# Performance work log

Hardware: AMD Instinct MI355X
Metric: run time of the kernel (lower is better)

## Reference

```python
import jax, jax.numpy as jnp
import numpy as np

N_NODES = 50000
N_EDGES = 800000
F_IN = 256
HID = 128
HEADS = 4
F_OUT = 64
NEG_SLOPE = 0.2


def setup_inputs() -> dict:
    key = jax.random.key(0)
    ks = jax.random.split(key, 12)
    x = jax.random.normal(ks[0], (N_NODES, F_IN), dtype=jnp.float32)
    edge_index = jax.random.randint(ks[1], (2, N_EDGES), 0, N_NODES, dtype=jnp.int64)
    s = 0.05
    return {
        "x": x,
        "edge_index": edge_index,
        "W1": jax.random.normal(ks[2], (F_IN, HEADS * HID), dtype=jnp.float32) * s,
        "a_src1": jax.random.normal(ks[3], (HEADS, HID), dtype=jnp.float32) * s,
        "a_dst1": jax.random.normal(ks[4], (HEADS, HID), dtype=jnp.float32) * s,
        "b1": jnp.zeros((HEADS * HID,), dtype=jnp.float32),
        "W2": jax.random.normal(ks[5], (HEADS * HID, F_OUT), dtype=jnp.float32) * s,
        "a_src2": jax.random.normal(ks[6], (1, F_OUT), dtype=jnp.float32) * s,
        "a_dst2": jax.random.normal(ks[7], (1, F_OUT), dtype=jnp.float32) * s,
        "b2": jnp.zeros((F_OUT,), dtype=jnp.float32),
    }


def _add_self_loops(edge_index, n):
    loop = jnp.arange(n, dtype=edge_index.dtype)
    return jnp.concatenate([edge_index, jnp.stack([loop, loop])], axis=1)


def _gat_conv(x, edge_index, W, a_src, a_dst, bias, heads, out_ch):
    # PyG GATConv: h = x @ W reshaped to [N, H, C]
    n = x.shape[0]
    h = (x @ W).reshape(n, heads, out_ch)
    # per-node attention logits [N, H]
    al_src = jnp.einsum('nhc,hc->nh', h, a_src)
    al_dst = jnp.einsum('nhc,hc->nh', h, a_dst)
    src, dst = edge_index[0], edge_index[1]
    e = jax.nn.leaky_relu(al_src[src] + al_dst[dst], NEG_SLOPE)  # [E, H]
    # softmax over incoming edges per destination node (segment softmax)
    e_max = jax.ops.segment_max(e, dst, num_segments=n)
    e_exp = jnp.exp(e - e_max[dst])
    denom = jax.ops.segment_sum(e_exp, dst, num_segments=n)
    alpha = e_exp / (denom[dst] + 1e-16)  # [E, H]
    msg = h[src] * alpha[:, :, None]  # [E, H, C]
    out = jax.ops.segment_sum(msg, dst, num_segments=n)  # [N, H, C]
    return out.reshape(n, heads * out_ch) + bias


def reference(x, edge_index, W1, a_src1, a_dst1, b1, W2, a_src2, a_dst2, b2):
    # Dropout layers are identity in eval mode.
    ei = _add_self_loops(edge_index, x.shape[0])
    h = jax.nn.elu(_gat_conv(x, ei, W1, a_src1, a_dst1, b1, HEADS, HID))
    out = _gat_conv(h, ei, W2, a_src2, a_dst2, b2, 1, F_OUT)
    return out
```

## Files before the change

### kernel.cpp

```cpp
#include <hip/hip_runtime.h>
#include <math.h>

#define N_NODES 50000
#define N_EDGES 800000
#define E_TOT   850000
#define F_IN    256
#define F1      512
#define HID     128
#define HEADS   4
#define F_OUT   64

typedef __attribute__((ext_vector_type(8))) short short8;
typedef __attribute__((ext_vector_type(4))) float f32x4;
typedef unsigned short ushort_t;
typedef unsigned int uint_t;

__device__ __forceinline__ float lrelu(float x){ return x > 0.f ? x : 0.2f*x; }
__device__ __forceinline__ float elu(float x){ return x > 0.f ? x : expm1f(x); }

__device__ __forceinline__ ushort_t f2b(float f){
  uint_t u = __builtin_bit_cast(uint_t, f);
  u += 0x7fffu + ((u >> 16) & 1u);
  return (ushort_t)(u >> 16);
}
__device__ __forceinline__ float blo(uint_t u){ return __builtin_bit_cast(float, u << 16); }
__device__ __forceinline__ float bhi(uint_t u){ return __builtin_bit_cast(float, u & 0xffff0000u); }
__device__ __forceinline__ float b2f(ushort_t s){ return __builtin_bit_cast(float, (uint_t)s << 16); }

__global__ void hist_kernel(const int* __restrict__ ei, int* __restrict__ deg){
  int e = blockIdx.x*blockDim.x + threadIdx.x;
  if (e >= E_TOT) return;
  int dst = (e < N_EDGES) ? ei[N_EDGES + e] : (e - N_EDGES);
  atomicAdd(&deg[dst], 1);
}

__global__ __launch_bounds__(256) void scan1_kernel(const int* __restrict__ deg,
                                                    int* __restrict__ offs,
                                                    int* __restrict__ bsum){
  __shared__ int sd[256];
  const int tid = threadIdx.x;
  const int i = blockIdx.x*256 + tid;
  int v = (i < N_NODES) ? deg[i] : 0;
  sd[tid] = v; __syncthreads();
  #pragma unroll
  for (int off = 1; off < 256; off <<= 1){
    int t = (tid >= off) ? sd[tid - off] : 0;
    __syncthreads();
    sd[tid] += t;
    __syncthreads();
  }
  if (i < N_NODES) offs[i] = sd[tid] - v;
  if (tid == 255) bsum[blockIdx.x] = sd[255];
}

__global__ __launch_bounds__(256) void scan2_kernel(const int* __restrict__ bsum,
                                                    int* __restrict__ bbase, int nb){
  __shared__ int sd[256];
  const int tid = threadIdx.x;
  int v = (tid < nb) ? bsum[tid] : 0;
  sd[tid] = v; __syncthreads();
  #pragma unroll
  for (int off = 1; off < 256; off <<= 1){
    int t = (tid >= off) ? sd[tid - off] : 0;
    __syncthreads();
    sd[tid] += t;
    __syncthreads();
  }
  if (tid < nb) bbase[tid] = sd[tid] - v;
}

__global__ __launch_bounds__(256) void scan3_kernel(int* __restrict__ offs,
                                                    const int* __restrict__ bbase,
                                                    int* __restrict__ cur){
  const int i = blockIdx.x*256 + threadIdx.x;
  if (i < N_NODES){
    int o = offs[i] + bbase[blockIdx.x];
    offs[i] = o;
    cur[i] = o;
  }
  if (blockIdx.x == 0 && threadIdx.x == 0) offs[N_NODES] = E_TOT;
}

__global__ void scatter_kernel(const int* __restrict__ ei, int* __restrict__ cur,
                               int* __restrict__ ssrc){
  int e = blockIdx.x*blockDim.x + threadIdx.x;
  if (e >= E_TOT) return;
  int src, dst;
  if (e < N_EDGES){ src = ei[e]; dst = ei[N_EDGES + e]; }
  else            { src = e - N_EDGES; dst = src; }
  int pos = atomicAdd(&cur[dst], 1);
  ssrc[pos] = src;
}

__global__ __launch_bounds__(256) void cvt_x_kernel(const float* __restrict__ x,
                                                    ushort_t* __restrict__ xb){
  const int t = blockIdx.x*256 + threadIdx.x;
  const float4 a = ((const float4*)x)[t*2];
  const float4 b = ((const float4*)x)[t*2 + 1];
  uint4 o;
  o.x = (uint_t)f2b(a.x) | ((uint_t)f2b(a.y) << 16);
  o.y = (uint_t)f2b(a.z) | ((uint_t)f2b(a.w) << 16);
  o.z = (uint_t)f2b(b.x) | ((uint_t)f2b(b.y) << 16);
  o.w = (uint_t)f2b(b.z) | ((uint_t)f2b(b.w) << 16);
  ((uint4*)xb)[t] = o;
}

__global__ __launch_bounds__(256) void transpose_bf16_kernel(const float* __restrict__ W,
                                                             ushort_t* __restrict__ Wt,
                                                             int K, int N){
  __shared__ float tile[64][65];
  const int k0 = blockIdx.x*64, n0 = blockIdx.y*64;
  const int c = threadIdx.x & 63, r4 = threadIdx.x >> 6;
  for (int r = r4; r < 64; r += 4)
    tile[r][c] = W[(size_t)(k0 + r)*N + n0 + c];
  __syncthreads();
  for (int r = r4; r < 64; r += 4)
    Wt[(size_t)(n0 + r)*K + k0 + c] = f2b(tile[c][r]);
}

template<int K, int WR, int WC>
__global__ __launch_bounds__(256) void gemm_bf16(const ushort_t* __restrict__ A,
                                                 const ushort_t* __restrict__ Bt,
                                                 ushort_t* __restrict__ C,
                                                 int M, int N){
  constexpr int BM = WR*64, BN = WC*64, BKP = 40;
  __shared__ ushort_t As[BM*BKP];
  __shared__ ushort_t Bs[BN*BKP];
  const int tid = threadIdx.x;
  const int wave = tid >> 6, lane = tid & 63, quad = lane >> 4, l16 = lane & 15;
  const int wm = wave % WR, wn = wave / WR;
  const int m0 = blockIdx.x*BM, n0 = blockIdx.y*BN;
  f32x4 acc[4][4] = {};
  for (int k0 = 0; k0 < K; k0 += 32){
    #pragma unroll
    for (int s = tid; s < BM*4; s += 256){
      int r = s >> 2, c = s & 3;
      int gr = m0 + r; if (gr >= M) gr = M - 1;
      *(uint4*)(As + r*BKP + c*8) = *(const uint4*)(A + (size_t)gr*K + k0 + c*8);
    }
    #pragma unroll
    for (int s = tid; s < BN*4; s += 256){
      int r = s >> 2, c = s & 3;
      *(uint4*)(Bs + r*BKP + c*8) = *(const uint4*)(Bt + (size_t)(n0 + r)*K + k0 + c*8);
    }
    __syncthreads();
    short8 af[4], bfr[4];
    #pragma unroll
    for (int i = 0; i < 4; ++i)
      af[i] = *(const short8*)(As + (wm*64 + i*16 + l16)*BKP + quad*8);
    #pragma unroll
    for (int j = 0; j < 4; ++j)
      bfr[j] = *(const short8*)(Bs + (wn*64 + j*16 + l16)*BKP + quad*8);
    #pragma unroll
    for (int i = 0; i < 4; ++i)
      #pragma unroll
      for (int j = 0; j < 4; ++j)
        acc[i][j] = __builtin_amdgcn_mfma_f32_16x16x32_bf16(af[i], bfr[j], acc[i][j], 0, 0, 0);
    __syncthreads();
  }
  #pragma unroll
  for (int i = 0; i < 4; ++i){
    #pragma unroll
    for (int r = 0; r < 4; ++r){
      int row = m0 + wm*64 + i*16 + quad*4 + r;
      if (row < M){
        #pragma unroll
        for (int j = 0; j < 4; ++j){
          int col = n0 + wn*64 + j*16 + l16;
          C[(size_t)row*N + col] = f2b(acc[i][j][r]);
        }
      }
    }
  }
}

__global__ __launch_bounds__(128) void logits1_kernel(const ushort_t* __restrict__ h1b,
                                                      const float* __restrict__ a_src,
                                                      const float* __restrict__ a_dst,
                                                      float* __restrict__ als,
                                                      float* __restrict__ ald){
  const int n = blockIdx.x;
  const int tid = threadIdx.x;
  const int head = tid >> 5, p = tid & 31;
  const uint2 v = *(const uint2*)(h1b + (size_t)n*F1 + tid*4);
  float h0 = blo(v.x), h1 = bhi(v.x), h2 = blo(v.y), h3 = bhi(v.y);
  const float4 as = *(const float4*)(a_src + head*HID + p*4);
  const float4 ad = *(const float4*)(a_dst + head*HID + p*4);
  float ds = h0*as.x + h1*as.y + h2*as.z + h3*as.w;
  float dd = h0*ad.x + h1*ad.y + h2*ad.z + h3*ad.w;
  #pragma unroll
  for (int off = 16; off >= 1; off >>= 1){
    ds += __shfl_down(ds, off, 32);
    dd += __shfl_down(dd, off, 32);
  }
  if (p == 0){ als[n*4 + head] = ds; ald[n*4 + head] = dd; }
}

#define FMA8(hv, al) do{ \
  acc[0] = fmaf(blo((hv).x), (al), acc[0]); \
  acc[1] = fmaf(bhi((hv).x), (al), acc[1]); \
  acc[2] = fmaf(blo((hv).y), (al), acc[2]); \
  acc[3] = fmaf(bhi((hv).y), (al), acc[3]); \
  acc[4] = fmaf(blo((hv).z), (al), acc[4]); \
  acc[5] = fmaf(bhi((hv).z), (al), acc[5]); \
  acc[6] = fmaf(blo((hv).w), (al), acc[6]); \
  acc[7] = fmaf(bhi((hv).w), (al), acc[7]); }while(0)

__global__ __launch_bounds__(256) void agg1_kernel(const ushort_t* __restrict__ h1b,
                                                   const float* __restrict__ als,
                                                   const float* __restrict__ ald1,
                                                   const float* __restrict__ b1,
                                                   const int* __restrict__ offs,
                                                   const int* __restrict__ ssrc,
                                                   ushort_t* __restrict__ hb){
  __shared__ int   shsrc[4][64];
  __shared__ float shal[4][64][4];
  const int wave = threadIdx.x >> 6, lane = threadIdx.x & 63;
  const int n = blockIdx.x*4 + wave;
  const int head = lane >> 4;
  const float4 ald = ((const float4*)ald1)[n];
  const int s0 = offs[n], s1 = offs[n+1];
  const int nE = s1 - s0;

  float acc[8] = {0.f,0.f,0.f,0.f,0.f,0.f,0.f,0.f};

  if (nE <= 64){
    float4 a4 = {0.f,0.f,0.f,0.f};
    int sc = 0;
    if (lane < nE){
      sc = ssrc[s0 + lane];
      const float4 as = ((const float4*)als)[sc];
      a4.x = __expf(lrelu(as.x + ald.x));
      a4.y = __expf(lrelu(as.y + ald.y));
      a4.z = __expf(lrelu(as.z + ald.z));
      a4.w = __expf(lrelu(as.w + ald.w));
    }
    shsrc[wave][lane] = sc;
    *(float4*)&shal[wave][lane][0] = a4;

    const ushort_t* hbase = h1b + lane*8;
    const int nE4 = (nE + 3) & ~3;
    float dsum = 0.f;

    uint4 h0  = *(const uint4*)(hbase + ((size_t)shsrc[wave][0] << 9));
    uint4 h1v = *(const uint4*)(hbase + ((size_t)shsrc[wave][1] << 9));
    uint4 h2v = *(const uint4*)(hbase + ((size_t)shsrc[wave][2] << 9));
    uint4 h3v = *(const uint4*)(hbase + ((size_t)shsrc[wave][3] << 9));
    float al0 = shal[wave][0][head];
    float al1 = shal[wave][1][head];
    float al2 = shal[wave][2][head];
    float al3 = shal[wave][3][head];
    for (int k = 0; k < nE4; k += 4){
      uint4 p0 = h0, p1 = h1v, p2 = h2v, p3 = h3v;
      float q0 = 0.f, q1 = 0.f, q2 = 0.f, q3 = 0.f;
      if (k + 4 < nE4){
        p0 = *(const uint4*)(hbase + ((size_t)shsrc[wave][k+4] << 9));
        p1 = *(const uint4*)(hbase + ((size_t)shsrc[wave][k+5] << 9));
        p2 = *(const uint4*)(hbase + ((size_t)shsrc[wave][k+6] << 9));
        p3 = *(const uint4*)(hbase + ((size_t)shsrc[wave][k+7] << 9));
        q0 = shal[wave][k+4][head];
        q1 = shal[wave][k+5][head];
        q2 = shal[wave][k+6][head];
        q3 = shal[wave][k+7][head];
      }
      dsum += (al0 + al1) + (al2 + al3);
      FMA8(h0,  al0);
      FMA8(h1v, al1);
      FMA8(h2v, al2);
      FMA8(h3v, al3);
      h0 = p0; h1v = p1; h2v = p2; h3v = p3;
      al0 = q0; al1 = q1; al2 = q2; al3 = q3;
    }

    const float rd = 1.0f / (dsum + 1e-16f);
    const float4 ba = *(const float4*)(b1 + lane*8);
    const float4 bb = *(const float4*)(b1 + lane*8 + 4);
    float o0 = elu(fmaf(acc[0], rd, ba.x)), o1 = elu(fmaf(acc[1], rd, ba.y));
    float o2 = elu(fmaf(acc[2], rd, ba.z)), o3 = elu(fmaf(acc[3], rd, ba.w));
    float o4 = elu(fmaf(acc[4], rd, bb.x)), o5 = elu(fmaf(acc[5], rd, bb.y));
    float o6 = elu(fmaf(acc[6], rd, bb.z)), o7 = elu(fmaf(acc[7], rd, bb.w));
    uint4 o;
    o.x = (uint_t)f2b(o0) | ((uint_t)f2b(o1) << 16);
    o.y = (uint_t)f2b(o2) | ((uint_t)f2b(o3) << 16);
    o.z = (uint_t)f2b(o4) | ((uint_t)f2b(o5) << 16);
    o.w = (uint_t)f2b(o6) | ((uint_t)f2b(o7) << 16);
    *(uint4*)(hb + (size_t)n*F1 + lane*8) = o;
    return;
  }

  float d0 = 0.f, d1 = 0.f, d2 = 0.f, d3 = 0.f;
  for (int e = s0 + lane; e < s1; e += 64){
    const int sc = ssrc[e];
    const float4 as = ((const float4*)als)[sc];
    d0 += __expf(lrelu(as.x + ald.x));
    d1 += __expf(lrelu(as.y + ald.y));
    d2 += __expf(lrelu(as.z + ald.z));
    d3 += __expf(lrelu(as.w + ald.w));
  }
  #pragma unroll
  for (int off = 32; off >= 1; off >>= 1){
    d0 += __shfl_xor(d0, off);
    d1 += __shfl_xor(d1, off);
    d2 += __shfl_xor(d2, off);
    d3 += __shfl_xor(d3, off);
  }
  const float den = (head == 0) ? d0 : (head == 1) ? d1 : (head == 2) ? d2 : d3;
  const float rd = 1.0f / (den + 1e-16f);

  for (int ce = s0; ce < s1; ce += 64){
    const int idx = ce + lane;
    if (idx < s1){
      const int sc = ssrc[idx];
      const float4 as = ((const float4*)als)[sc];
      shsrc[wave][lane] = sc;
      float4 a4;
      a4.x = __expf(lrelu(as.x + ald.x));
      a4.y = __expf(lrelu(as.y + ald.y));
      a4.z = __expf(lrelu(as.z + ald.z));
      a4.w = __expf(lrelu(as.w + ald.w));
      *(float4*)&shal[wave][lane][0] = a4;
    }
    const int nB = min(64, s1 - ce);
    for (int k = 0; k < nB; ++k){
      const int scb = shsrc[wave][k];
      const float al = shal[wave][k][head] * rd;
      const uint4 hv = *(const uint4*)(h1b + (size_t)scb*F1 + lane*8);
      FMA8(hv, al);
    }
  }
  const float4 ba = *(const float4*)(b1 + lane*8);
  const float4 bb = *(const float4*)(b1 + lane*8 + 4);
  float o0 = elu(acc[0] + ba.x), o1 = elu(acc[1] + ba.y);
  float o2 = elu(acc[2] + ba.z), o3 = elu(acc[3] + ba.w);
  float o4 = elu(acc[4] + bb.x), o5 = elu(acc[5] + bb.y);
  float o6 = elu(acc[6] + bb.z), o7 = elu(acc[7] + bb.w);
  uint4 o;
  o.x = (uint_t)f2b(o0) | ((uint_t)f2b(o1) << 16);
  o.y = (uint_t)f2b(o2) | ((uint_t)f2b(o3) << 16);
  o.z = (uint_t)f2b(o4) | ((uint_t)f2b(o5) << 16);
  o.w = (uint_t)f2b(o6) | ((uint_t)f2b(o7) << 16);
  *(uint4*)(hb + (size_t)n*F1 + lane*8) = o;
}

__global__ __launch_bounds__(64) void logits2_kernel(const ushort_t* __restrict__ gb,
                                                     const float* __restrict__ a_src,
                                                     const float* __restrict__ a_dst,
                                                     float* __restrict__ als,
                                                     float* __restrict__ ald){
  const int n = blockIdx.x;
  const int tid = threadIdx.x;
  const float v = b2f(gb[(size_t)n*F_OUT + tid]);
  float ds = v * a_src[tid];
  float dd = v * a_dst[tid];
  #pragma unroll
  for (int off = 32; off >= 1; off >>= 1){
    ds += __shfl_xor(ds, off);
    dd += __shfl_xor(dd, off);
  }
  if (tid == 0){ als[n] = ds; ald[n] = dd; }
}

__global__ __launch_bounds__(256) void agg2_kernel(const ushort_t* __restrict__ gb,
                                                   const float* __restrict__ als,
                                                   const float* __restrict__ ald2,
                                                   const float* __restrict__ b2,
                                                   const int* __restrict__ offs,
                                                   const int* __restrict__ ssrc,
                                                   float* __restrict__ out){
  __shared__ int   shsrc[4][64];
  __shared__ float shal[4][64];
  const int wave = threadIdx.x >> 6, lane = threadIdx.x & 63;
  const int n = blockIdx.x*4 + wave;
  const float ald = ald2[n];
  const int s0 = offs[n], s1 = offs[n+1];
  const int nE = s1 - s0;

  if (nE <= 64){
    float av = 0.f; int sc = 0;
    if (lane < nE){
      sc = ssrc[s0 + lane];
      av = __expf(lrelu(als[sc] + ald));
    }
    shsrc[wave][lane] = sc;
    shal[wave][lane] = av;

    const ushort_t* gbase = gb + lane;
    const int nE4 = (nE + 3) & ~3;
    float acc = 0.f, dsum = 0.f;

    ushort_t v0 = gbase[(size_t)shsrc[wave][0] << 6];
    ushort_t v1 = gbase[(size_t)shsrc[wave][1] << 6];
    ushort_t v2 = gbase[(size_t)shsrc[wave][2] << 6];
    ushort_t v3 = gbase[(size_t)shsrc[wave][3] << 6];
    float al0 = shal[wave][0];
    float al1 = shal[wave][1];
    float al2 = shal[wave][2];
    float al3 = shal[wave][3];
    for (int k = 0; k < nE4; k += 4){
      ushort_t p0 = v0, p1 = v1, p2 = v2, p3 = v3;
      float q0 = 0.f, q1 = 0.f, q2 = 0.f, q3 = 0.f;
      if (k + 4 < nE4){
        p0 = gbase[(size_t)shsrc[wave][k+4] << 6];
        p1 = gbase[(size_t)shsrc[wave][k+5] << 6];
        p2 = gbase[(size_t)shsrc[wave][k+6] << 6];
        p3 = gbase[(size_t)shsrc[wave][k+7] << 6];
        q0 = shal[wave][k+4];
        q1 = shal[wave][k+5];
        q2 = shal[wave][k+6];
        q3 = shal[wave][k+7];
      }
      dsum += (al0 + al1) + (al2 + al3);
      acc = fmaf(b2f(v0), al0, acc);
      acc = fmaf(b2f(v1), al1, acc);
      acc = fmaf(b2f(v2), al2, acc);
      acc = fmaf(b2f(v3), al3, acc);
      v0 = p0; v1 = p1; v2 = p2; v3 = p3;
      al0 = q0; al1 = q1; al2 = q2; al3 = q3;
    }
    const float rd = 1.0f / (dsum + 1e-16f);
    out[(size_t)n*F_OUT + lane] = fmaf(acc, rd, b2[lane]);
    return;
  }

  float dsum = 0.f;
  for (int e = s0 + lane; e < s1; e += 64)
    dsum += __expf(lrelu(als[ssrc[e]] + ald));
  #pragma unroll
  for (int off = 32; off >= 1; off >>= 1)
    dsum += __shfl_xor(dsum, off);
  const float rd = 1.0f / (dsum + 1e-16f);

  float acc = 0.f;
  for (int ce = s0; ce < s1; ce += 64){
    const int idx = ce + lane;
    if (idx < s1){
      const int sc = ssrc[idx];
      shsrc[wave][lane] = sc;
      shal[wave][lane] = __expf(lrelu(als[sc] + ald)) * rd;
    }
    const int nB = min(64, s1 - ce);
    for (int k = 0; k < nB; ++k){
      const int scb = shsrc[wave][k];
      const float al = shal[wave][k];
      acc = fmaf(b2f(gb[(size_t)scb*F_OUT + lane]), al, acc);
    }
  }
  out[(size_t)n*F_OUT + lane] = acc + b2[lane];
}

#undef FMA8

extern "C" void kernel_launch(void* const* d_in, const int* in_sizes, int n_in,
                              void* d_out, int out_size, void* d_ws, size_t ws_size,
                              hipStream_t stream){
  const float* x      = (const float*)d_in[0];
  const int*   ei     = (const int*)  d_in[1];
  const float* W1     = (const float*)d_in[2];
  const float* a_src1 = (const float*)d_in[3];
  const float* a_dst1 = (const float*)d_in[4];
  const float* b1     = (const float*)d_in[5];
  const float* W2     = (const float*)d_in[6];
  const float* a_src2 = (const float*)d_in[7];
  const float* a_dst2 = (const float*)d_in[8];
  const float* b2     = (const float*)d_in[9];
  float* out = (float*)d_out;

  char* ws = (char*)d_ws;
  ushort_t* h1b  = (ushort_t*)(ws + 0UL);
  ushort_t* hb   = (ushort_t*)(ws + 51200000UL);
  ushort_t* xb   = (ushort_t*)(ws + 102400000UL);
  ushort_t* gb   = (ushort_t*)(ws + 128000000UL);
  ushort_t* W1t  = (ushort_t*)(ws + 134400000UL);
  ushort_t* W2t  = (ushort_t*)(ws + 134662144UL);
  float*    als1 = (float*)   (ws + 134727680UL);
  float*    ald1 = (float*)   (ws + 135527680UL);
  float*    als2 = (float*)   (ws + 136327680UL);
  float*    ald2 = (float*)   (ws + 136527680UL);
  int*      deg  = (int*)     (ws + 136727680UL);
  int*      offs = (int*)     (ws + 136927680UL);
  int*      bsum = (int*)     (ws + 137127744UL);
  int*      bbase= (int*)     (ws + 137128544UL);
  int*      cur  = (int*)     (ws + 137129600UL);
  int*      ssrc = (int*)     (ws + 137329600UL);

  hipMemsetAsync(deg, 0, 200000, stream);

  const int eb = (E_TOT + 255) / 256;
  const int nb = (N_NODES + 255) / 256;
  hist_kernel   <<<eb, 256, 0, stream>>>(ei, deg);
  scan1_kernel  <<<nb, 256, 0, stream>>>(deg, offs, bsum);
  scan2_kernel  <<<1, 256, 0, stream>>>(bsum, bbase, nb);
  scan3_kernel  <<<nb, 256, 0, stream>>>(offs, bbase, cur);
  scatter_kernel<<<eb, 256, 0, stream>>>(ei, cur, ssrc);

  cvt_x_kernel        <<<6250, 256, 0, stream>>>(x, xb);
  transpose_bf16_kernel<<<dim3(4, 8), 256, 0, stream>>>(W1, W1t, F_IN, F1);
  transpose_bf16_kernel<<<dim3(8, 1), 256, 0, stream>>>(W2, W2t, F1, F_OUT);

  gemm_bf16<F_IN, 2, 2><<<dim3(391, 4), 256, 0, stream>>>(xb, W1t, h1b, N_NODES, F1);
  logits1_kernel<<<N_NODES, 128, 0, stream>>>(h1b, a_src1, a_dst1, als1, ald1);
  agg1_kernel   <<<12500, 256, 0, stream>>>(h1b, als1, ald1, b1, offs, ssrc, hb);

  gemm_bf16<F1, 4, 1><<<dim3(196, 1), 256, 0, stream>>>(hb, W2t, gb, N_NODES, F_OUT);
  logits2_kernel<<<N_NODES, 64, 0, stream>>>(gb, a_src2, a_dst2, als2, ald2);
  agg2_kernel   <<<12500, 256, 0, stream>>>(gb, als2, ald2, b2, offs, ssrc, out);
}
```

Before: 469.5 us.

## Fuse attention logit computation into GEMM epilogues and drop logits kernels

Computes the per-node source and destination attention logits directly from the fp32 MFMA accumulators in the GEMM epilogue, removing the two separate logits kernels and their re-reads of h1/g. Layer 1 changes the GEMM tile to 64x256 so each wave owns a half head, and combines the two halves with atomicAdd into zeroed buffers. The memset is widened to clear the logit buffers along with deg. Logits now come from unrounded fp32 values rather than bf16, and the float atomics make summation order nondeterministic.

New measurement: 489.3 us. 1.04x slower.

```diff
diff --git a/kernel.cpp b/kernel.cpp
--- a/kernel.cpp
+++ b/kernel.cpp
@@ -118,11 +118,15 @@
     Wt[(size_t)(n0 + r)*K + k0 + c] = f2b(tile[c][r]);
 }
 
-template<int K, int WR, int WC>
+template<int K, int WR, int WC, int MODE>
 __global__ __launch_bounds__(256) void gemm_bf16(const ushort_t* __restrict__ A,
                                                  const ushort_t* __restrict__ Bt,
                                                  ushort_t* __restrict__ C,
-                                                 int M, int N){
+                                                 int M, int N,
+                                                 const float* __restrict__ eas,
+                                                 const float* __restrict__ ead,
+                                                 float* __restrict__ oas,
+                                                 float* __restrict__ oad){
   constexpr int BM = WR*64, BN = WC*64, BKP = 40;
   __shared__ ushort_t As[BM*BKP];
   __shared__ ushort_t Bs[BN*BKP];
@@ -172,28 +176,74 @@
       }
     }
   }
-}
-
-__global__ __launch_bounds__(128) void logits1_kernel(const ushort_t* __restrict__ h1b,
-                                                      const float* __restrict__ a_src,
-                                                      const float* __restrict__ a_dst,
-                                                      float* __restrict__ als,
-                                                      float* __restrict__ ald){
-  const int n = blockIdx.x;
-  const int tid = threadIdx.x;
-  const int head = tid >> 5, p = tid & 31;
-  const uint2 v = *(const uint2*)(h1b + (size_t)n*F1 + tid*4);
-  float h0 = blo(v.x), h1 = bhi(v.x), h2 = blo(v.y), h3 = bhi(v.y);
-  const float4 as = *(const float4*)(a_src + head*HID + p*4);
-  const float4 ad = *(const float4*)(a_dst + head*HID + p*4);
-  float ds = h0*as.x + h1*as.y + h2*as.z + h3*as.w;
-  float dd = h0*ad.x + h1*ad.y + h2*ad.z + h3*ad.w;
-  #pragma unroll
-  for (int off = 16; off >= 1; off >>= 1){
-    ds += __shfl_down(ds, off, 32);
-    dd += __shfl_down(dd, off, 32);
-  }
-  if (p == 0){ als[n*4 + head] = ds; ald[n*4 + head] = dd; }
+
+  if constexpr (MODE == 1){
+    const int head = (n0 + wn*64) >> 7;
+    const int cbase = head*HID + (wn & 1)*64;
+    float as_[4], ad_[4];
+    #pragma unroll
+    for (int j = 0; j < 4; ++j){
+      as_[j] = eas[cbase + j*16 + l16];
+      ad_[j] = ead[cbase + j*16 + l16];
+    }
+    #pragma unroll
+    for (int i = 0; i < 4; ++i){
+      #pragma unroll
+      for (int r = 0; r < 4; ++r){
+        float s = 0.f, d = 0.f;
+        #pragma unroll
+        for (int j = 0; j < 4; ++j){
+          s = fmaf(acc[i][j][r], as_[j], s);
+          d = fmaf(acc[i][j][r], ad_[j], d);
+        }
+        #pragma unroll
+        for (int off = 8; off >= 1; off >>= 1){
+          s += __shfl_xor(s, off);
+          d += __shfl_xor(d, off);
+        }
+        if (l16 == 0){
+          int row = m0 + wm*64 + i*16 + quad*4 + r;
+          if (row < M){
+            atomicAdd(&oas[row*4 + head], s);
+            atomicAdd(&oad[row*4 + head], d);
+          }
+        }
+      }
+    }
+  }
+
+  if constexpr (MODE == 2){
+    float as_[4], ad_[4];
+    #pragma unroll
+    for (int j = 0; j < 4; ++j){
+      as_[j] = eas[j*16 + l16];
+      ad_[j] = ead[j*16 + l16];
+    }
+    #pragma unroll
+    for (int i = 0; i < 4; ++i){
+      #pragma unroll
+      for (int r = 0; r < 4; ++r){
+        float s = 0.f, d = 0.f;
+        #pragma unroll
+        for (int j = 0; j < 4; ++j){
+          s = fmaf(acc[i][j][r], as_[j], s);
+          d = fmaf(acc[i][j][r], ad_[j], d);
+        }
+        #pragma unroll
+        for (int off = 8; off >= 1; off >>= 1){
+          s += __shfl_xor(s, off);
+          d += __shfl_xor(d, off);
+        }
+        if (l16 == 0){
+          int row = m0 + wm*64 + i*16 + quad*4 + r;
+          if (row < M){
+            oas[row] = s;
+            oad[row] = d;
+          }
+        }
+      }
+    }
+  }
 }
 
 #define FMA8(hv, al) do{ \
@@ -342,24 +392,6 @@
   *(uint4*)(hb + (size_t)n*F1 + lane*8) = o;
 }
 
-__global__ __launch_bounds__(64) void logits2_kernel(const ushort_t* __restrict__ gb,
-                                                     const float* __restrict__ a_src,
-                                                     const float* __restrict__ a_dst,
-                                                     float* __restrict__ als,
-                                                     float* __restrict__ ald){
-  const int n = blockIdx.x;
-  const int tid = threadIdx.x;
-  const float v = b2f(gb[(size_t)n*F_OUT + tid]);
-  float ds = v * a_src[tid];
-  float dd = v * a_dst[tid];
-  #pragma unroll
-  for (int off = 32; off >= 1; off >>= 1){
-    ds += __shfl_xor(ds, off);
-    dd += __shfl_xor(dd, off);
-  }
-  if (tid == 0){ als[n] = ds; ald[n] = dd; }
-}
-
 __global__ __launch_bounds__(256) void agg2_kernel(const ushort_t* __restrict__ gb,
                                                    const float* __restrict__ als,
                                                    const float* __restrict__ ald2,
@@ -483,7 +515,7 @@
   int*      cur  = (int*)     (ws + 137129600UL);
   int*      ssrc = (int*)     (ws + 137329600UL);
 
-  hipMemsetAsync(deg, 0, 200000, stream);
+  hipMemsetAsync(als1, 0, 2200000, stream);
 
   const int eb = (E_TOT + 255) / 256;
   const int nb = (N_NODES + 255) / 256;
@@ -497,11 +529,11 @@
   transpose_bf16_kernel<<<dim3(4, 8), 256, 0, stream>>>(W1, W1t, F_IN, F1);
   transpose_bf16_kernel<<<dim3(8, 1), 256, 0, stream>>>(W2, W2t, F1, F_OUT);
 
-  gemm_bf16<F_IN, 2, 2><<<dim3(391, 4), 256, 0, stream>>>(xb, W1t, h1b, N_NODES, F1);
-  logits1_kernel<<<N_NODES, 128, 0, stream>>>(h1b, a_src1, a_dst1, als1, ald1);
-  agg1_kernel   <<<12500, 256, 0, stream>>>(h1b, als1, ald1, b1, offs, ssrc, hb);
-
-  gemm_bf16<F1, 4, 1><<<dim3(196, 1), 256, 0, stream>>>(hb, W2t, gb, N_NODES, F_OUT);
-  logits2_kernel<<<N_NODES, 64, 0, stream>>>(gb, a_src2, a_dst2, als2, ald2);
-  agg2_kernel   <<<12500, 256, 0, stream>>>(gb, als2, ald2, b2, offs, ssrc, out);
-}
+  gemm_bf16<F_IN, 1, 4, 1><<<dim3(782, 2), 256, 0, stream>>>(
+      xb, W1t, h1b, N_NODES, F1, a_src1, a_dst1, als1, ald1);
+  agg1_kernel<<<12500, 256, 0, stream>>>(h1b, als1, ald1, b1, offs, ssrc, hb);
+
+  gemm_bf16<F1, 4, 1, 2><<<dim3(196, 1), 256, 0, stream>>>(
+      hb, W2t, gb, N_NODES, F_OUT, a_src2, a_dst2, als2, ald2);
+  agg2_kernel<<<12500, 256, 0, stream>>>(gb, als2, ald2, b2, offs, ssrc, out);
+}
```

## Pad degree/cursor counters to 64B and split agg2 edges across half-waves

Applied to the files above, without the earlier changes.

The per-node degree and cursor counters are spread to one int per 64-byte stride, so atomics on neighbouring nodes no longer share a cache line. The buffers move into the hb workspace region, which is still free at that point. The layer-2 aggregation's short-degree path now has each half-wave handle alternate edges, with every lane loading two bf16 channels as one 32-bit word, and the halves are combined by a shuffle. The aim is less atomic contention and fewer scalar 16-bit gather loads, at the cost of more memory for the counters and a lost software prefetch.

New measurement: 475.2 us. No clear change (+1.2%).

```diff
diff --git a/kernel.cpp b/kernel.cpp
--- a/kernel.cpp
+++ b/kernel.cpp
@@ -27,20 +27,20 @@
 __device__ __forceinline__ float bhi(uint_t u){ return __builtin_bit_cast(float, u & 0xffff0000u); }
 __device__ __forceinline__ float b2f(ushort_t s){ return __builtin_bit_cast(float, (uint_t)s << 16); }
 
-__global__ void hist_kernel(const int* __restrict__ ei, int* __restrict__ deg){
+__global__ void hist_kernel(const int* __restrict__ ei, int* __restrict__ deg16){
   int e = blockIdx.x*blockDim.x + threadIdx.x;
   if (e >= E_TOT) return;
   int dst = (e < N_EDGES) ? ei[N_EDGES + e] : (e - N_EDGES);
-  atomicAdd(&deg[dst], 1);
-}
-
-__global__ __launch_bounds__(256) void scan1_kernel(const int* __restrict__ deg,
+  atomicAdd(&deg16[dst*16], 1);
+}
+
+__global__ __launch_bounds__(256) void scan1_kernel(const int* __restrict__ deg16,
                                                     int* __restrict__ offs,
                                                     int* __restrict__ bsum){
   __shared__ int sd[256];
   const int tid = threadIdx.x;
   const int i = blockIdx.x*256 + tid;
-  int v = (i < N_NODES) ? deg[i] : 0;
+  int v = (i < N_NODES) ? deg16[i*16] : 0;
   sd[tid] = v; __syncthreads();
   #pragma unroll
   for (int off = 1; off < 256; off <<= 1){
@@ -71,24 +71,24 @@
 
 __global__ __launch_bounds__(256) void scan3_kernel(int* __restrict__ offs,
                                                     const int* __restrict__ bbase,
-                                                    int* __restrict__ cur){
+                                                    int* __restrict__ cur16){
   const int i = blockIdx.x*256 + threadIdx.x;
   if (i < N_NODES){
     int o = offs[i] + bbase[blockIdx.x];
     offs[i] = o;
-    cur[i] = o;
+    cur16[i*16] = o;
   }
   if (blockIdx.x == 0 && threadIdx.x == 0) offs[N_NODES] = E_TOT;
 }
 
-__global__ void scatter_kernel(const int* __restrict__ ei, int* __restrict__ cur,
+__global__ void scatter_kernel(const int* __restrict__ ei, int* __restrict__ cur16,
                                int* __restrict__ ssrc){
   int e = blockIdx.x*blockDim.x + threadIdx.x;
   if (e >= E_TOT) return;
   int src, dst;
   if (e < N_EDGES){ src = ei[e]; dst = ei[N_EDGES + e]; }
   else            { src = e - N_EDGES; dst = src; }
-  int pos = atomicAdd(&cur[dst], 1);
+  int pos = atomicAdd(&cur16[dst*16], 1);
   ssrc[pos] = src;
 }
 
@@ -384,41 +384,28 @@
     shsrc[wave][lane] = sc;
     shal[wave][lane] = av;
 
-    const ushort_t* gbase = gb + lane;
-    const int nE4 = (nE + 3) & ~3;
-    float acc = 0.f, dsum = 0.f;
-
-    ushort_t v0 = gbase[(size_t)shsrc[wave][0] << 6];
-    ushort_t v1 = gbase[(size_t)shsrc[wave][1] << 6];
-    ushort_t v2 = gbase[(size_t)shsrc[wave][2] << 6];
-    ushort_t v3 = gbase[(size_t)shsrc[wave][3] << 6];
-    float al0 = shal[wave][0];
-    float al1 = shal[wave][1];
-    float al2 = shal[wave][2];
-    float al3 = shal[wave][3];
-    for (int k = 0; k < nE4; k += 4){
-      ushort_t p0 = v0, p1 = v1, p2 = v2, p3 = v3;
-      float q0 = 0.f, q1 = 0.f, q2 = 0.f, q3 = 0.f;
-      if (k + 4 < nE4){
-        p0 = gbase[(size_t)shsrc[wave][k+4] << 6];
-        p1 = gbase[(size_t)shsrc[wave][k+5] << 6];
-        p2 = gbase[(size_t)shsrc[wave][k+6] << 6];
-        p3 = gbase[(size_t)shsrc[wave][k+7] << 6];
-        q0 = shal[wave][k+4];
-        q1 = shal[wave][k+5];
-        q2 = shal[wave][k+6];
-        q3 = shal[wave][k+7];
-      }
-      dsum += (al0 + al1) + (al2 + al3);
-      acc = fmaf(b2f(v0), al0, acc);
-      acc = fmaf(b2f(v1), al1, acc);
-      acc = fmaf(b2f(v2), al2, acc);
-      acc = fmaf(b2f(v3), al3, acc);
-      v0 = p0; v1 = p1; v2 = p2; v3 = p3;
-      al0 = q0; al1 = q1; al2 = q2; al3 = q3;
-    }
+    const int half = lane >> 5;
+    const int ch2  = lane & 31;
+    float acc0 = 0.f, acc1 = 0.f, dsum = 0.f;
+    for (int k = half; k < nE; k += 2){
+      const int scb  = shsrc[wave][k];
+      const float al = shal[wave][k];
+      const uint_t v = *(const uint_t*)(gb + ((size_t)scb << 6) + ch2*2);
+      acc0 = fmaf(blo(v), al, acc0);
+      acc1 = fmaf(bhi(v), al, acc1);
+      dsum += al;
+    }
+    acc0 += __shfl_xor(acc0, 32);
+    acc1 += __shfl_xor(acc1, 32);
+    dsum += __shfl_xor(dsum, 32);
     const float rd = 1.0f / (dsum + 1e-16f);
-    out[(size_t)n*F_OUT + lane] = fmaf(acc, rd, b2[lane]);
+    if (lane < 32){
+      const float2 bb = *(const float2*)(b2 + ch2*2);
+      float2 o2;
+      o2.x = fmaf(acc0, rd, bb.x);
+      o2.y = fmaf(acc1, rd, bb.y);
+      *(float2*)(out + (size_t)n*F_OUT + ch2*2) = o2;
+    }
     return;
   }
 
@@ -476,22 +463,23 @@
   float*    ald1 = (float*)   (ws + 135527680UL);
   float*    als2 = (float*)   (ws + 136327680UL);
   float*    ald2 = (float*)   (ws + 136527680UL);
-  int*      deg  = (int*)     (ws + 136727680UL);
   int*      offs = (int*)     (ws + 136927680UL);
   int*      bsum = (int*)     (ws + 137127744UL);
   int*      bbase= (int*)     (ws + 137128544UL);
-  int*      cur  = (int*)     (ws + 137129600UL);
   int*      ssrc = (int*)     (ws + 137329600UL);
 
-  hipMemsetAsync(deg, 0, 200000, stream);
+  int*      deg16 = (int*)    (ws + 51200000UL);
+  int*      cur16 = (int*)    (ws + 54400000UL);
+
+  hipMemsetAsync(deg16, 0, 3200000, stream);
 
   const int eb = (E_TOT + 255) / 256;
   const int nb = (N_NODES + 255) / 256;
-  hist_kernel   <<<eb, 256, 0, stream>>>(ei, deg);
-  scan1_kernel  <<<nb, 256, 0, stream>>>(deg, offs, bsum);
+  hist_kernel   <<<eb, 256, 0, stream>>>(ei, deg16);
+  scan1_kernel  <<<nb, 256, 0, stream>>>(deg16, offs, bsum);
   scan2_kernel  <<<1, 256, 0, stream>>>(bsum, bbase, nb);
-  scan3_kernel  <<<nb, 256, 0, stream>>>(offs, bbase, cur);
-  scatter_kernel<<<eb, 256, 0, stream>>>(ei, cur, ssrc);
+  scan3_kernel  <<<nb, 256, 0, stream>>>(offs, bbase, cur16);
+  scatter_kernel<<<eb, 256, 0, stream>>>(ei, cur16, ssrc);
 
   cvt_x_kernel        <<<6250, 256, 0, stream>>>(x, xb);
   transpose_bf16_kernel<<<dim3(4, 8), 256, 0, stream>>>(W1, W1t, F_IN, F1);
```

## Split layer-1 aggregation into column slices with 8 nodes per wave

Applied to the files above, without the earlier changes.

The layer-1 aggregation kernel is rewritten so that each block handles one 64-column slice (half a head) for 32 nodes. Each wave processes 8 nodes with 8 lanes per node, rather than one whole 512-wide node per wave. Work is divided by column slice across blocks, which aims to improve L2 locality of gathered h1 rows and to load-balance low-degree nodes instead of leaving most of a 64-lane wave idle. In exchange, attention logits and exponentials are recomputed per slice, each gather is only 128 bytes, and there are extra LDS exchanges. The separate high-degree path is removed.

New measurement: 446.9 us. 4.8% less time.

```diff
diff --git a/kernel.cpp b/kernel.cpp
--- a/kernel.cpp
+++ b/kernel.cpp
@@ -206,75 +206,61 @@
   acc[6] = fmaf(blo((hv).w), (al), acc[6]); \
   acc[7] = fmaf(bhi((hv).w), (al), acc[7]); }while(0)
 
-__global__ __launch_bounds__(256) void agg1_kernel(const ushort_t* __restrict__ h1b,
-                                                   const float* __restrict__ als,
-                                                   const float* __restrict__ ald1,
-                                                   const float* __restrict__ b1,
-                                                   const int* __restrict__ offs,
-                                                   const int* __restrict__ ssrc,
-                                                   ushort_t* __restrict__ hb){
-  __shared__ int   shsrc[4][64];
-  __shared__ float shal[4][64][4];
+__global__ __launch_bounds__(256) void agg1s_kernel(const ushort_t* __restrict__ h1b,
+                                                    const float* __restrict__ als,
+                                                    const float* __restrict__ ald1,
+                                                    const float* __restrict__ b1,
+                                                    const int* __restrict__ offs,
+                                                    const int* __restrict__ ssrc,
+                                                    ushort_t* __restrict__ hb){
+  __shared__ int   shsrc[4][8][8];
+  __shared__ float shal[4][8][8];
   const int wave = threadIdx.x >> 6, lane = threadIdx.x & 63;
-  const int n = blockIdx.x*4 + wave;
-  const int head = lane >> 4;
-  const float4 ald = ((const float4*)ald1)[n];
-  const int s0 = offs[n], s1 = offs[n+1];
-  const int nE = s1 - s0;
-
+  const int s = blockIdx.x & 7;
+  const int gblk = blockIdx.x >> 3;
+  const int head = s >> 1;
+  const int g  = lane >> 3;
+  const int l8 = lane & 7;
+  const int n = gblk*32 + wave*8 + g;
+  const bool valid = n < N_NODES;
+
+  const int s0  = valid ? offs[n]     : 0;
+  const int s1v = valid ? offs[n + 1] : 0;
+  const int nE  = s1v - s0;
+  const float aldv = valid ? ald1[n*4 + head] : 0.f;
+
+  const ushort_t* hcol = h1b + s*64 + l8*8;
   float acc[8] = {0.f,0.f,0.f,0.f,0.f,0.f,0.f,0.f};
-
-  if (nE <= 64){
-    float4 a4 = {0.f,0.f,0.f,0.f};
-    int sc = 0;
-    if (lane < nE){
-      sc = ssrc[s0 + lane];
-      const float4 as = ((const float4*)als)[sc];
-      a4.x = __expf(lrelu(as.x + ald.x));
-      a4.y = __expf(lrelu(as.y + ald.y));
-      a4.z = __expf(lrelu(as.z + ald.z));
-      a4.w = __expf(lrelu(as.w + ald.w));
-    }
-    shsrc[wave][lane] = sc;
-    *(float4*)&shal[wave][lane][0] = a4;
-
-    const ushort_t* hbase = h1b + lane*8;
-    const int nE4 = (nE + 3) & ~3;
-    float dsum = 0.f;
-
-    uint4 h0  = *(const uint4*)(hbase + ((size_t)shsrc[wave][0] << 9));
-    uint4 h1v = *(const uint4*)(hbase + ((size_t)shsrc[wave][1] << 9));
-    uint4 h2v = *(const uint4*)(hbase + ((size_t)shsrc[wave][2] << 9));
-    uint4 h3v = *(const uint4*)(hbase + ((size_t)shsrc[wave][3] << 9));
-    float al0 = shal[wave][0][head];
-    float al1 = shal[wave][1][head];
-    float al2 = shal[wave][2][head];
-    float al3 = shal[wave][3][head];
-    for (int k = 0; k < nE4; k += 4){
-      uint4 p0 = h0, p1 = h1v, p2 = h2v, p3 = h3v;
-      float q0 = 0.f, q1 = 0.f, q2 = 0.f, q3 = 0.f;
-      if (k + 4 < nE4){
-        p0 = *(const uint4*)(hbase + ((size_t)shsrc[wave][k+4] << 9));
-        p1 = *(const uint4*)(hbase + ((size_t)shsrc[wave][k+5] << 9));
-        p2 = *(const uint4*)(hbase + ((size_t)shsrc[wave][k+6] << 9));
-        p3 = *(const uint4*)(hbase + ((size_t)shsrc[wave][k+7] << 9));
-        q0 = shal[wave][k+4][head];
-        q1 = shal[wave][k+5][head];
-        q2 = shal[wave][k+6][head];
-        q3 = shal[wave][k+7][head];
-      }
-      dsum += (al0 + al1) + (al2 + al3);
-      FMA8(h0,  al0);
-      FMA8(h1v, al1);
-      FMA8(h2v, al2);
-      FMA8(h3v, al3);
-      h0 = p0; h1v = p1; h2v = p2; h3v = p3;
-      al0 = q0; al1 = q1; al2 = q2; al3 = q3;
-    }
-
+  float dsum = 0.f;
+
+  const int nC = (nE + 7) >> 3;
+  for (int c = 0; c < nC; ++c){
+    const int idx = s0 + c*8 + l8;
+    int sc = 0; float a = 0.f;
+    if (idx < s1v){
+      sc = ssrc[idx];
+      a  = __expf(lrelu(als[sc*4 + head] + aldv));
+    }
+    shsrc[wave][g][l8] = sc;
+    shal[wave][g][l8]  = a;
+    dsum += a;
+    #pragma unroll
+    for (int k = 0; k < 8; ++k){
+      const int scb  = shsrc[wave][g][k];
+      const float al = shal[wave][g][k];
+      const uint4 v = *(const uint4*)(hcol + ((size_t)scb << 9));
+      FMA8(v, al);
+    }
+  }
+
+  dsum += __shfl_xor(dsum, 1);
+  dsum += __shfl_xor(dsum, 2);
+  dsum += __shfl_xor(dsum, 4);
+
+  if (valid){
     const float rd = 1.0f / (dsum + 1e-16f);
-    const float4 ba = *(const float4*)(b1 + lane*8);
-    const float4 bb = *(const float4*)(b1 + lane*8 + 4);
+    const float4 ba = *(const float4*)(b1 + s*64 + l8*8);
+    const float4 bb = *(const float4*)(b1 + s*64 + l8*8 + 4);
     float o0 = elu(fmaf(acc[0], rd, ba.x)), o1 = elu(fmaf(acc[1], rd, ba.y));
     float o2 = elu(fmaf(acc[2], rd, ba.z)), o3 = elu(fmaf(acc[3], rd, ba.w));
     float o4 = elu(fmaf(acc[4], rd, bb.x)), o5 = elu(fmaf(acc[5], rd, bb.y));
@@ -284,62 +270,8 @@
     o.y = (uint_t)f2b(o2) | ((uint_t)f2b(o3) << 16);
     o.z = (uint_t)f2b(o4) | ((uint_t)f2b(o5) << 16);
     o.w = (uint_t)f2b(o6) | ((uint_t)f2b(o7) << 16);
-    *(uint4*)(hb + (size_t)n*F1 + lane*8) = o;
-    return;
-  }
-
-  float d0 = 0.f, d1 = 0.f, d2 = 0.f, d3 = 0.f;
-  for (int e = s0 + lane; e < s1; e += 64){
-    const int sc = ssrc[e];
-    const float4 as = ((const float4*)als)[sc];
-    d0 += __expf(lrelu(as.x + ald.x));
-    d1 += __expf(lrelu(as.y + ald.y));
-    d2 += __expf(lrelu(as.z + ald.z));
-    d3 += __expf(lrelu(as.w + ald.w));
-  }
-  #pragma unroll
-  for (int off = 32; off >= 1; off >>= 1){
-    d0 += __shfl_xor(d0, off);
-    d1 += __shfl_xor(d1, off);
-    d2 += __shfl_xor(d2, off);
-    d3 += __shfl_xor(d3, off);
-  }
-  const float den = (head == 0) ? d0 : (head == 1) ? d1 : (head == 2) ? d2 : d3;
-  const float rd = 1.0f / (den + 1e-16f);
-
-  for (int ce = s0; ce < s1; ce += 64){
-    const int idx = ce + lane;
-    if (idx < s1){
-      const int sc = ssrc[idx];
-      const float4 as = ((const float4*)als)[sc];
-      shsrc[wave][lane] = sc;
-      float4 a4;
-      a4.x = __expf(lrelu(as.x + ald.x));
-      a4.y = __expf(lrelu(as.y + ald.y));
-      a4.z = __expf(lrelu(as.z + ald.z));
-      a4.w = __expf(lrelu(as.w + ald.w));
-      *(float4*)&shal[wave][lane][0] = a4;
-    }
-    const int nB = min(64, s1 - ce);
-    for (int k = 0; k < nB; ++k){
-      const int scb = shsrc[wave][k];
-      const float al = shal[wave][k][head] * rd;
-      const uint4 hv = *(const uint4*)(h1b + (size_t)scb*F1 + lane*8);
-      FMA8(hv, al);
-    }
-  }
-  const float4 ba = *(const float4*)(b1 + lane*8);
-  const float4 bb = *(const float4*)(b1 + lane*8 + 4);
-  float o0 = elu(acc[0] + ba.x), o1 = elu(acc[1] + ba.y);
-  float o2 = elu(acc[2] + ba.z), o3 = elu(acc[3] + ba.w);
-  float o4 = elu(acc[4] + bb.x), o5 = elu(acc[5] + bb.y);
-  float o6 = elu(acc[6] + bb.z), o7 = elu(acc[7] + bb.w);
-  uint4 o;
-  o.x = (uint_t)f2b(o0) | ((uint_t)f2b(o1) << 16);
-  o.y = (uint_t)f2b(o2) | ((uint_t)f2b(o3) << 16);
-  o.z = (uint_t)f2b(o4) | ((uint_t)f2b(o5) << 16);
-  o.w = (uint_t)f2b(o6) | ((uint_t)f2b(o7) << 16);
-  *(uint4*)(hb + (size_t)n*F1 + lane*8) = o;
+    *(uint4*)(hb + (size_t)n*F1 + s*64 + l8*8) = o;
+  }
 }
 
 __global__ __launch_bounds__(64) void logits2_kernel(const ushort_t* __restrict__ gb,
@@ -499,7 +431,7 @@
 
   gemm_bf16<F_IN, 2, 2><<<dim3(391, 4), 256, 0, stream>>>(xb, W1t, h1b, N_NODES, F1);
   logits1_kernel<<<N_NODES, 128, 0, stream>>>(h1b, a_src1, a_dst1, als1, ald1);
-  agg1_kernel   <<<12500, 256, 0, stream>>>(h1b, als1, ald1, b1, offs, ssrc, hb);
+  agg1s_kernel  <<<12504, 256, 0, stream>>>(h1b, als1, ald1, b1, offs, ssrc, hb);
 
   gemm_bf16<F1, 4, 1><<<dim3(196, 1), 256, 0, stream>>>(hb, W2t, gb, N_NODES, F_OUT);
   logits2_kernel<<<N_NODES, 64, 0, stream>>>(gb, a_src2, a_dst2, als2, ald2);
```
